# Kernel tuning notes

Measured on AMD Instinct MI355X. Metric: run time of the kernel, lower is better.

The kernel has to match this reference:

```python
import jax, jax.numpy as jnp
import numpy as np

N_NODES = 100000
N_EDGES = 3200000
N_FEAT = 128
N_GRAPHS = 64


def setup_inputs() -> dict:
    key = jax.random.key(0)
    ks = jax.random.split(key, 8)
    x = jax.random.normal(ks[0], (N_NODES, N_FEAT), dtype=jnp.float32)
    edge_index = jax.random.randint(ks[1], (2, N_EDGES), 0, N_NODES, dtype=jnp.int64)
    batch = jnp.sort(jax.random.randint(ks[2], (N_NODES,), 0, N_GRAPHS, dtype=jnp.int64))
    # GCNConv weights (glorot-style scale) and biases
    W1 = jax.random.normal(ks[3], (N_FEAT, 32), dtype=jnp.float32) / np.sqrt(N_FEAT)
    b1 = jnp.zeros((32,), dtype=jnp.float32)
    W2 = jax.random.normal(ks[4], (32, 16), dtype=jnp.float32) / np.sqrt(32.0)
    b2 = jnp.zeros((16,), dtype=jnp.float32)
    lin_w = jax.random.normal(ks[5], (16, 1), dtype=jnp.float32) / np.sqrt(16.0)
    lin_b = jnp.zeros((1,), dtype=jnp.float32)
    return {"x": x, "edge_index": edge_index, "batch": batch,
            "W1": W1, "b1": b1, "W2": W2, "b2": b2,
            "lin_w": lin_w, "lin_b": lin_b}


def _gcn_conv(x, W, b, src, dst, deg_inv_sqrt, n_nodes):
    # transform first (fewer features downstream when out_dim < in_dim)
    xw = x @ W  # [N, out]
    norm = deg_inv_sqrt[src] * deg_inv_sqrt[dst]  # [E+N]
    msg = xw[src] * norm[:, None]  # gather + scale
    out = jax.ops.segment_sum(msg, dst, num_segments=n_nodes)  # scatter-add
    return out + b


def reference(x, edge_index, batch, W1, b1, W2, b2, lin_w, lin_b):
    n_nodes = x.shape[0]
    self_loop = jnp.arange(n_nodes, dtype=edge_index.dtype)
    src = jnp.concatenate([edge_index[0], self_loop])
    dst = jnp.concatenate([edge_index[1], self_loop])
    # symmetric GCN normalization with self-loops
    deg = jax.ops.segment_sum(jnp.ones_like(src, dtype=x.dtype), dst,
                              num_segments=n_nodes)
    deg_inv_sqrt = jnp.where(deg > 0, jax.lax.rsqrt(jnp.maximum(deg, 1.0)), 0.0)

    h = _gcn_conv(x, W1, b1, src, dst, deg_inv_sqrt, n_nodes)
    h = jax.nn.relu(h)
    # F.dropout with training=False (eval) is identity
    h = _gcn_conv(h, W2, b2, src, dst, deg_inv_sqrt, n_nodes)

    # global_mean_pool over batch index
    sums = jax.ops.segment_sum(h, batch, num_segments=N_GRAPHS)  # [G,16]
    cnts = jax.ops.segment_sum(jnp.ones((n_nodes,), dtype=h.dtype), batch,
                               num_segments=N_GRAPHS)
    pooled = sums / jnp.maximum(cnts, 1.0)[:, None]
    return pooled @ lin_w + lin_b  # [G,1]
```

## Files before the change

### kernel.cpp

```cpp
#include <hip/hip_runtime.h>

#define NN 100000
#define NE 3200000
#define NF 128
#define C1 32
#define C2 16
#define NG 64
#define BKT_SH 7
#define BKT_W  128
#define NBKT   782
#define CH     8192
#define NW     391
#define RSTR   784
#define MAPCAP 6400

#define OFF_BCNT  0
#define OFF_BST   1024
#define OFF_RUN   2048
#define OFF_ROW   308608
#define OFF_DIS   408624
#define OFF_POOL  508624
#define OFF_CNTF  509648
#define OFF_EDG   509712
#define OFF_XS1B  OFF_EDG
#define OFF_H1    (OFF_EDG + NE)
#define OFF_XS2B  (OFF_H1  + NN*C1)
#define OFF_H2    (OFF_XS2B + NN*8)
#define OFF_COL   (OFF_H2  + NN*C2)

__device__ __forceinline__ unsigned pack_bf2(float a, float b) {
    unsigned ua = __float_as_uint(a);
    unsigned ub = __float_as_uint(b);
    ua = (ua + 0x7fffu + ((ua >> 16) & 1u)) >> 16;
    ub = (ub + 0x7fffu + ((ub >> 16) & 1u)) & 0xffff0000u;
    return ua | ub;
}
__device__ __forceinline__ float2 unpack_bf2(unsigned u) {
    return make_float2(__uint_as_float(u << 16), __uint_as_float(u & 0xffff0000u));
}

__global__ __launch_bounds__(256) void k_part(
    const int* __restrict__ S, const int* __restrict__ D,
    unsigned* __restrict__ edgebuf, int* __restrict__ runstart,
    int* __restrict__ bcnt)
{
    __shared__ int lhist[1024];
    __shared__ int lstart[1024];
    __shared__ int lcur[NBKT];
    __shared__ int sd[256];
    __shared__ unsigned lsort[CH];
    const int w = blockIdx.x;
    const int t = threadIdx.x;
    const int e0 = w * CH;
    const int n = min(CH, NE - e0);

    for (int i = t; i < 1024; i += 256) lhist[i] = 0;
    __syncthreads();
    for (int i = t; i < n; i += 256)
        atomicAdd(&lhist[(unsigned)D[e0 + i] >> BKT_SH], 1);
    __syncthreads();
    for (int i = t; i < NBKT; i += 256) atomicAdd(&bcnt[i], lhist[i]);
    int c0 = lhist[t * 4 + 0], c1 = lhist[t * 4 + 1];
    int c2 = lhist[t * 4 + 2], c3 = lhist[t * 4 + 3];
    int ts = c0 + c1 + c2 + c3;
    sd[t] = ts;
    __syncthreads();
    for (int off = 1; off < 256; off <<= 1) {
        int v = (t >= off) ? sd[t - off] : 0;
        __syncthreads();
        sd[t] += v;
        __syncthreads();
    }
    int excl = sd[t] - ts;
    lstart[t * 4 + 0] = excl;
    lstart[t * 4 + 1] = excl + c0;
    lstart[t * 4 + 2] = excl + c0 + c1;
    lstart[t * 4 + 3] = excl + c0 + c1 + c2;
    __syncthreads();
    for (int i = t; i < 783; i += 256) runstart[w * RSTR + i] = lstart[i];
    for (int i = t; i < NBKT; i += 256) lcur[i] = lstart[i];
    __syncthreads();
    for (int i = t; i < n; i += 256) {
        int s = S[e0 + i], d = D[e0 + i];
        int pos = atomicAdd(&lcur[(unsigned)d >> BKT_SH], 1);
        lsort[pos] = ((unsigned)s << BKT_SH) | (unsigned)(d & (BKT_W - 1));
    }
    __syncthreads();
    for (int i = t; i < n; i += 256) edgebuf[e0 + i] = lsort[i];
}

__global__ __launch_bounds__(256) void k_bscan(const int* __restrict__ bcnt,
                                               int* __restrict__ bstart,
                                               int* __restrict__ rowstart) {
    __shared__ int sd[256];
    const int t = threadIdx.x;
    const int base = t * 4;
    int c0 = (base + 0 < NBKT) ? bcnt[base + 0] : 0;
    int c1 = (base + 1 < NBKT) ? bcnt[base + 1] : 0;
    int c2 = (base + 2 < NBKT) ? bcnt[base + 2] : 0;
    int c3 = (base + 3 < NBKT) ? bcnt[base + 3] : 0;
    int ts = c0 + c1 + c2 + c3;
    sd[t] = ts;
    __syncthreads();
    for (int off = 1; off < 256; off <<= 1) {
        int v = (t >= off) ? sd[t - off] : 0;
        __syncthreads();
        sd[t] += v;
        __syncthreads();
    }
    int excl = sd[t] - ts;
    if (base + 0 < 783) bstart[base + 0] = excl;
    if (base + 1 < 783) bstart[base + 1] = excl + c0;
    if (base + 2 < 783) bstart[base + 2] = excl + c0 + c1;
    if (base + 3 < 783) bstart[base + 3] = excl + c0 + c1 + c2;
    if (t == 0) rowstart[NN] = NE;
}

__global__ __launch_bounds__(256) void k_fillfused(
    const unsigned* __restrict__ edgebuf, const int* __restrict__ runstart,
    const int* __restrict__ bstart,
    int* __restrict__ rowstart, float* __restrict__ dis, int* __restrict__ colidx)
{
    __shared__ int rl[NW];
    __shared__ int pfx[NW];
    __shared__ int basea[NW];
    __shared__ unsigned short map[MAPCAP];
    __shared__ int lcnt[BKT_W];
    __shared__ int lcur[BKT_W];
    __shared__ int sd[256];
    const int b = blockIdx.x;
    const int t = threadIdx.x;
    const int bs = bstart[b];
    const int total = bstart[b + 1] - bs;

    for (int w = t; w < NW; w += 256) {
        int s0 = runstart[w * RSTR + b];
        int s1 = runstart[w * RSTR + b + 1];
        basea[w] = s0;
        rl[w] = s1 - s0;
    }
    if (t < BKT_W) lcnt[t] = 0;
    __syncthreads();
    {
        int w0 = t * 2;
        int c0 = (w0 < NW) ? rl[w0] : 0;
        int c1 = (w0 + 1 < NW) ? rl[w0 + 1] : 0;
        int ts = c0 + c1;
        sd[t] = ts;
        __syncthreads();
        for (int off = 1; off < 256; off <<= 1) {
            int v = (t >= off) ? sd[t - off] : 0;
            __syncthreads();
            sd[t] += v;
            __syncthreads();
        }
        int excl = sd[t] - ts;
        if (w0 < NW)     pfx[w0]     = excl;
        if (w0 + 1 < NW) pfx[w0 + 1] = excl + c0;
    }
    __syncthreads();
    for (int w = t; w < NW; w += 256) {
        int p = pfx[w], len = rl[w];
        basea[w] = w * CH + basea[w] - p;
        for (int i = 0; i < len; ++i) map[p + i] = (unsigned short)w;
    }
    __syncthreads();
    for (int j = t; j < total; j += 256) {
        unsigned p = edgebuf[basea[map[j]] + j];
        atomicAdd(&lcnt[p & (BKT_W - 1)], 1);
    }
    __syncthreads();
    if (t < BKT_W) lcur[t] = lcnt[t];
    __syncthreads();
    for (int off = 1; off < BKT_W; off <<= 1) {
        int v = (t < BKT_W && t >= off) ? lcur[t - off] : 0;
        __syncthreads();
        if (t < BKT_W) lcur[t] += v;
        __syncthreads();
    }
    if (t < BKT_W) {
        int excl = lcur[t] - lcnt[t];
        int node = b * BKT_W + t;
        if (node < NN) {
            rowstart[node] = bs + excl;
            dis[node] = rsqrtf((float)lcnt[t] + 1.0f);
        }
        lcur[t] = bs + excl;
    }
    __syncthreads();
    for (int j = t; j < total; j += 256) {
        unsigned p = edgebuf[basea[map[j]] + j];
        int pos = atomicAdd(&lcur[p & (BKT_W - 1)], 1);
        colidx[pos] = (int)(p >> BKT_SH);
    }
}

__global__ __launch_bounds__(256) void k_gemm1(
    const float* __restrict__ x, const float* __restrict__ W1,
    const float* __restrict__ dis, unsigned* __restrict__ xs1b)
{
    __shared__ float xls[128 * 33];
    __shared__ float wls[32 * 32];
    const int t = threadIdx.x;
    const int tc = t & 7;
    const int tr = t >> 3;
    const int base = blockIdx.x * 128;

    float a[4][4] = {};

    for (int k0 = 0; k0 < NF; k0 += 32) {
        {
            int i = t * 4;
            int kk = i >> 5, c = i & 31;
            *(float4*)&wls[kk * 32 + c] = *(const float4*)&W1[(k0 + kk) * C1 + c];
        }
        #pragma unroll
        for (int r = 0; r < 4; ++r) {
            int n = (t >> 3) + r * 32;
            int j = (t & 7) * 4;
            int node = base + n;
            float4 v = make_float4(0.f, 0.f, 0.f, 0.f);
            if (node < NN) v = *(const float4*)&x[(long long)node * NF + k0 + j];
            xls[n * 33 + j + 0] = v.x;
            xls[n * 33 + j + 1] = v.y;
            xls[n * 33 + j + 2] = v.z;
            xls[n * 33 + j + 3] = v.w;
        }
        __syncthreads();
        #pragma unroll 8
        for (int kk = 0; kk < 32; ++kk) {
            float4 w = *(const float4*)&wls[kk * 32 + tc * 4];
            #pragma unroll
            for (int i = 0; i < 4; ++i) {
                float xv = xls[(tr * 4 + i) * 33 + kk];
                a[i][0] = fmaf(xv, w.x, a[i][0]);
                a[i][1] = fmaf(xv, w.y, a[i][1]);
                a[i][2] = fmaf(xv, w.z, a[i][2]);
                a[i][3] = fmaf(xv, w.w, a[i][3]);
            }
        }
        __syncthreads();
    }
    #pragma unroll
    for (int i = 0; i < 4; ++i) {
        int node = base + tr * 4 + i;
        if (node < NN) {
            float dv = dis[node];
            uint2 o;
            o.x = pack_bf2(a[i][0] * dv, a[i][1] * dv);
            o.y = pack_bf2(a[i][2] * dv, a[i][3] * dv);
            *(uint2*)&xs1b[node * 16 + tc * 2] = o;
        }
    }
}

__global__ __launch_bounds__(256) void k_gather1(
    const unsigned* __restrict__ xs1b, const int* __restrict__ colidx,
    const int* __restrict__ rowstart, const float* __restrict__ dis,
    const float* __restrict__ b1, float* __restrict__ h1)
{
    const int l = threadIdx.x & 15;
    const int v = blockIdx.x * 16 + (threadIdx.x >> 4);
    if (v >= NN) return;
    const int start = rowstart[v];
    const int num = rowstart[v + 1] - start;
    const int* __restrict__ cp = &colidx[start];

    float2 a0 = unpack_bf2(xs1b[v * 16 + l]);
    float2 a1 = make_float2(0.f, 0.f), a2 = a1, a3 = a1;
    int i = 0;
    for (; i + 4 <= num; i += 4) {
        int s0 = cp[i], s1 = cp[i + 1], s2 = cp[i + 2], s3 = cp[i + 3];
        float2 u0 = unpack_bf2(xs1b[s0 * 16 + l]);
        float2 u1 = unpack_bf2(xs1b[s1 * 16 + l]);
        float2 u2 = unpack_bf2(xs1b[s2 * 16 + l]);
        float2 u3 = unpack_bf2(xs1b[s3 * 16 + l]);
        a0.x += u0.x; a0.y += u0.y;
        a1.x += u1.x; a1.y += u1.y;
        a2.x += u2.x; a2.y += u2.y;
        a3.x += u3.x; a3.y += u3.y;
    }
    for (; i < num; ++i) {
        float2 u = unpack_bf2(xs1b[cp[i] * 16 + l]);
        a0.x += u.x; a0.y += u.y;
    }
    float accx = (a0.x + a1.x) + (a2.x + a3.x);
    float accy = (a0.y + a1.y) + (a2.y + a3.y);
    float dv = dis[v];
    float2 bv = *(const float2*)&b1[l * 2];
    float2 o;
    o.x = fmaxf(fmaf(accx, dv, bv.x), 0.f);
    o.y = fmaxf(fmaf(accy, dv, bv.y), 0.f);
    *(float2*)&h1[v * C1 + l * 2] = o;
}

__global__ __launch_bounds__(256) void k_gemm2(
    const float* __restrict__ h1, const float* __restrict__ W2,
    const float* __restrict__ dis, unsigned* __restrict__ xs2b)
{
    __shared__ float hls[128 * 33];
    __shared__ float wls[32 * 16];
    const int t = threadIdx.x;
    const int base = blockIdx.x * 128;

    if (t < 128) *(float4*)&wls[t * 4] = *(const float4*)&W2[t * 4];

    #pragma unroll
    for (int r = 0; r < 4; ++r) {
        int n = (t >> 3) + r * 32;
        int j = (t & 7) * 4;
        int node = base + n;
        float4 v = make_float4(0.f, 0.f, 0.f, 0.f);
        if (node < NN) v = *(const float4*)&h1[node * C1 + j];
        hls[n * 33 + j + 0] = v.x;
        hls[n * 33 + j + 1] = v.y;
        hls[n * 33 + j + 2] = v.z;
        hls[n * 33 + j + 3] = v.w;
    }
    __syncthreads();

    const int tc = t & 3;
    const int tr = t >> 2;
    float a[2][4] = {};
    #pragma unroll 8
    for (int kk = 0; kk < 32; ++kk) {
        float4 w = *(const float4*)&wls[kk * C2 + tc * 4];
        #pragma unroll
        for (int i = 0; i < 2; ++i) {
            float xv = hls[(tr * 2 + i) * 33 + kk];
            a[i][0] = fmaf(xv, w.x, a[i][0]);
            a[i][1] = fmaf(xv, w.y, a[i][1]);
            a[i][2] = fmaf(xv, w.z, a[i][2]);
            a[i][3] = fmaf(xv, w.w, a[i][3]);
        }
    }
    #pragma unroll
    for (int i = 0; i < 2; ++i) {
        int node = base + tr * 2 + i;
        if (node < NN) {
            float dv = dis[node];
            uint2 o;
            o.x = pack_bf2(a[i][0] * dv, a[i][1] * dv);
            o.y = pack_bf2(a[i][2] * dv, a[i][3] * dv);
            *(uint2*)&xs2b[node * 8 + tc * 2] = o;
        }
    }
}

__global__ __launch_bounds__(256) void k_gather2(
    const unsigned* __restrict__ xs2b, const int* __restrict__ colidx,
    const int* __restrict__ rowstart, const float* __restrict__ dis,
    const float* __restrict__ b2, float* __restrict__ h2)
{
    const int l = threadIdx.x & 7;
    const int v = blockIdx.x * 32 + (threadIdx.x >> 3);
    if (v >= NN) return;
    const int start = rowstart[v];
    const int num = rowstart[v + 1] - start;
    const int* __restrict__ cp = &colidx[start];

    float2 a0 = unpack_bf2(xs2b[v * 8 + l]);
    float2 a1 = make_float2(0.f, 0.f), a2 = a1, a3 = a1;
    int i = 0;
    for (; i + 4 <= num; i += 4) {
        int s0 = cp[i], s1 = cp[i + 1], s2 = cp[i + 2], s3 = cp[i + 3];
        float2 u0 = unpack_bf2(xs2b[s0 * 8 + l]);
        float2 u1 = unpack_bf2(xs2b[s1 * 8 + l]);
        float2 u2 = unpack_bf2(xs2b[s2 * 8 + l]);
        float2 u3 = unpack_bf2(xs2b[s3 * 8 + l]);
        a0.x += u0.x; a0.y += u0.y;
        a1.x += u1.x; a1.y += u1.y;
        a2.x += u2.x; a2.y += u2.y;
        a3.x += u3.x; a3.y += u3.y;
    }
    for (; i < num; ++i) {
        float2 u = unpack_bf2(xs2b[cp[i] * 8 + l]);
        a0.x += u.x; a0.y += u.y;
    }
    float accx = (a0.x + a1.x) + (a2.x + a3.x);
    float accy = (a0.y + a1.y) + (a2.y + a3.y);
    float dv = dis[v];
    float2 bv = *(const float2*)&b2[l * 2];
    float2 o;
    o.x = fmaf(accx, dv, bv.x);
    o.y = fmaf(accy, dv, bv.y);
    *(float2*)&h2[v * C2 + l * 2] = o;
}

__global__ __launch_bounds__(256) void k_pool(
    const float* __restrict__ h2, const int* __restrict__ batch,
    float* __restrict__ pool, float* __restrict__ cntf)
{
    __shared__ float ps[NG * C2];
    __shared__ float cs[NG];
    const int t = threadIdx.x;
    for (int i = t; i < NG * C2; i += 256) ps[i] = 0.f;
    if (t < NG) cs[t] = 0.f;
    __syncthreads();

    int v = blockIdx.x * 256 + t;
    if (v < NN) {
        int g = batch[v];
        atomicAdd(&cs[g], 1.0f);
        #pragma unroll
        for (int c = 0; c < C2; ++c)
            atomicAdd(&ps[g * C2 + c], h2[v * C2 + c]);
    }
    __syncthreads();
    for (int i = t; i < NG * C2; i += 256)
        if (ps[i] != 0.f) atomicAdd(&pool[i], ps[i]);
    if (t < NG && cs[t] != 0.f) atomicAdd(&cntf[t], cs[t]);
}

__global__ void k_final(const float* __restrict__ pool, const float* __restrict__ cntf,
                        const float* __restrict__ lw, const float* __restrict__ lb,
                        float* __restrict__ out)
{
    int g = threadIdx.x;
    if (g < NG) {
        float c = fmaxf(cntf[g], 1.0f);
        float inv = 1.0f / c;
        float s = lb[0];
        #pragma unroll
        for (int k = 0; k < C2; ++k) s = fmaf(pool[g * C2 + k] * inv, lw[k], s);
        out[g] = s;
    }
}

extern "C" void kernel_launch(void* const* d_in, const int* in_sizes, int n_in,
                              void* d_out, int out_size, void* d_ws, size_t ws_size,
                              hipStream_t stream) {
    const float* x     = (const float*)d_in[0];
    const int*   ei    = (const int*)d_in[1];
    const int*   batch = (const int*)d_in[2];
    const float* W1    = (const float*)d_in[3];
    const float* b1    = (const float*)d_in[4];
    const float* W2    = (const float*)d_in[5];
    const float* b2    = (const float*)d_in[6];
    const float* lw    = (const float*)d_in[7];
    const float* lb    = (const float*)d_in[8];
    float* out = (float*)d_out;

    float*    wsf = (float*)d_ws;
    int*      wsi = (int*)d_ws;
    unsigned* wsu = (unsigned*)d_ws;

    int*      bcnt     = wsi + OFF_BCNT;
    int*      bstart   = wsi + OFF_BST;
    int*      runstart = wsi + OFF_RUN;
    int*      rowstart = wsi + OFF_ROW;
    float*    dis      = wsf + OFF_DIS;
    float*    pool     = wsf + OFF_POOL;
    float*    cntf     = wsf + OFF_CNTF;
    unsigned* edgebuf  = wsu + OFF_EDG;
    unsigned* xs1b     = wsu + OFF_XS1B;
    float*    h1       = wsf + OFF_H1;
    unsigned* xs2b     = wsu + OFF_XS2B;
    float*    h2       = wsf + OFF_H2;
    int*      colidx   = wsi + OFF_COL;

    const int* S = ei;
    const int* D = ei + NE;

    hipMemsetAsync(bcnt, 0, 1024 * sizeof(int), stream);
    hipMemsetAsync(pool, 0, (NG * C2 + NG) * sizeof(float), stream);

    k_part     <<<NW, 256, 0, stream>>>(S, D, edgebuf, runstart, bcnt);
    k_bscan    <<<1, 256, 0, stream>>>(bcnt, bstart, rowstart);
    k_fillfused<<<NBKT, 256, 0, stream>>>(edgebuf, runstart, bstart, rowstart, dis, colidx);
    k_gemm1    <<<(NN + 127) / 128, 256, 0, stream>>>(x, W1, dis, xs1b);
    k_gather1  <<<(NN + 15) / 16, 256, 0, stream>>>(xs1b, colidx, rowstart, dis, b1, h1);
    k_gemm2    <<<(NN + 127) / 128, 256, 0, stream>>>(h1, W2, dis, xs2b);
    k_gather2  <<<(NN + 31) / 32, 256, 0, stream>>>(xs2b, colidx, rowstart, dis, b2, h2);
    k_pool     <<<(NN + 255) / 256, 256, 0, stream>>>(h2, batch, pool, cntf);
    k_final    <<<1, 64, 0, stream>>>(pool, cntf, lw, lb, out);
}
```

Before: 296.4 us.

## Split layer-1 gather into feature halves and fuse pooling into layer-2 gather

Layer-1 transformed features are stored as two separate 16-channel bf16 arrays, and the gather runs as two passes, each touching a 3.2 MB table instead of a 6.4 MB one. The aim is to keep the randomly gathered working set resident in cache. The cost is reading the column index list twice. Separately, the layer-2 gather now accumulates straight into shared-memory pooling sums, which removes the h2 buffer and the separate pool kernel at the price of more shared atomics inside the gather.

```diff
diff --git a/kernel.cpp b/kernel.cpp
--- a/kernel.cpp
+++ b/kernel.cpp
@@ -22,11 +22,12 @@
 #define OFF_POOL  508624
 #define OFF_CNTF  509648
 #define OFF_EDG   509712
-#define OFF_XS1B  OFF_EDG
-#define OFF_H1    (OFF_EDG + NE)
-#define OFF_XS2B  (OFF_H1  + NN*C1)
-#define OFF_H2    (OFF_XS2B + NN*8)
-#define OFF_COL   (OFF_H2  + NN*C2)
+#define OFF_XS1H0 OFF_EDG
+#define OFF_XS1H1 (OFF_EDG + NN*8)
+#define OFF_H1A   (OFF_EDG + NE)
+#define OFF_H1B   (OFF_H1A + NN*16)
+#define OFF_XS2B  (OFF_H1B + NN*16)
+#define OFF_COL   (OFF_XS2B + NN*8)
 
 __device__ __forceinline__ unsigned pack_bf2(float a, float b) {
     unsigned ua = __float_as_uint(a);
@@ -197,7 +198,8 @@
 
 __global__ __launch_bounds__(256) void k_gemm1(
     const float* __restrict__ x, const float* __restrict__ W1,
-    const float* __restrict__ dis, unsigned* __restrict__ xs1b)
+    const float* __restrict__ dis,
+    unsigned* __restrict__ xs1h0, unsigned* __restrict__ xs1h1)
 {
     __shared__ float xls[128 * 33];
     __shared__ float wls[32 * 32];
@@ -249,53 +251,57 @@
             uint2 o;
             o.x = pack_bf2(a[i][0] * dv, a[i][1] * dv);
             o.y = pack_bf2(a[i][2] * dv, a[i][3] * dv);
-            *(uint2*)&xs1b[node * 16 + tc * 2] = o;
-        }
-    }
-}
-
-__global__ __launch_bounds__(256) void k_gather1(
-    const unsigned* __restrict__ xs1b, const int* __restrict__ colidx,
+            unsigned* dst = (tc < 4) ? &xs1h0[node * 8 + tc * 2]
+                                     : &xs1h1[node * 8 + (tc - 4) * 2];
+            *(uint2*)dst = o;
+        }
+    }
+}
+
+template<int HALF>
+__global__ __launch_bounds__(256) void k_gather1h(
+    const unsigned* __restrict__ xsh, const int* __restrict__ colidx,
     const int* __restrict__ rowstart, const float* __restrict__ dis,
-    const float* __restrict__ b1, float* __restrict__ h1)
-{
-    const int l = threadIdx.x & 15;
-    const int v = blockIdx.x * 16 + (threadIdx.x >> 4);
+    const float* __restrict__ b1, float* __restrict__ h1h)
+{
+    const int l = threadIdx.x & 7;
+    const int v = blockIdx.x * 32 + (threadIdx.x >> 3);
     if (v >= NN) return;
     const int start = rowstart[v];
     const int num = rowstart[v + 1] - start;
     const int* __restrict__ cp = &colidx[start];
 
-    float2 a0 = unpack_bf2(xs1b[v * 16 + l]);
+    float2 a0 = unpack_bf2(xsh[v * 8 + l]);
     float2 a1 = make_float2(0.f, 0.f), a2 = a1, a3 = a1;
     int i = 0;
     for (; i + 4 <= num; i += 4) {
         int s0 = cp[i], s1 = cp[i + 1], s2 = cp[i + 2], s3 = cp[i + 3];
-        float2 u0 = unpack_bf2(xs1b[s0 * 16 + l]);
-        float2 u1 = unpack_bf2(xs1b[s1 * 16 + l]);
-        float2 u2 = unpack_bf2(xs1b[s2 * 16 + l]);
-        float2 u3 = unpack_bf2(xs1b[s3 * 16 + l]);
+        float2 u0 = unpack_bf2(xsh[s0 * 8 + l]);
+        float2 u1 = unpack_bf2(xsh[s1 * 8 + l]);
+        float2 u2 = unpack_bf2(xsh[s2 * 8 + l]);
+        float2 u3 = unpack_bf2(xsh[s3 * 8 + l]);
         a0.x += u0.x; a0.y += u0.y;
         a1.x += u1.x; a1.y += u1.y;
         a2.x += u2.x; a2.y += u2.y;
         a3.x += u3.x; a3.y += u3.y;
     }
     for (; i < num; ++i) {
-        float2 u = unpack_bf2(xs1b[cp[i] * 16 + l]);
+        float2 u = unpack_bf2(xsh[cp[i] * 8 + l]);
         a0.x += u.x; a0.y += u.y;
     }
     float accx = (a0.x + a1.x) + (a2.x + a3.x);
     float accy = (a0.y + a1.y) + (a2.y + a3.y);
     float dv = dis[v];
-    float2 bv = *(const float2*)&b1[l * 2];
+    float2 bv = *(const float2*)&b1[HALF * 16 + l * 2];
     float2 o;
     o.x = fmaxf(fmaf(accx, dv, bv.x), 0.f);
     o.y = fmaxf(fmaf(accy, dv, bv.y), 0.f);
-    *(float2*)&h1[v * C1 + l * 2] = o;
+    *(float2*)&h1h[v * 16 + l * 2] = o;
 }
 
 __global__ __launch_bounds__(256) void k_gemm2(
-    const float* __restrict__ h1, const float* __restrict__ W2,
+    const float* __restrict__ h1a, const float* __restrict__ h1b,
+    const float* __restrict__ W2,
     const float* __restrict__ dis, unsigned* __restrict__ xs2b)
 {
     __shared__ float hls[128 * 33];
@@ -311,7 +317,10 @@
         int j = (t & 7) * 4;
         int node = base + n;
         float4 v = make_float4(0.f, 0.f, 0.f, 0.f);
-        if (node < NN) v = *(const float4*)&h1[node * C1 + j];
+        if (node < NN) {
+            v = (j < 16) ? *(const float4*)&h1a[node * 16 + j]
+                         : *(const float4*)&h1b[node * 16 + (j - 16)];
+        }
         hls[n * 33 + j + 0] = v.x;
         hls[n * 33 + j + 1] = v.y;
         hls[n * 33 + j + 2] = v.z;
@@ -350,65 +359,53 @@
 __global__ __launch_bounds__(256) void k_gather2(
     const unsigned* __restrict__ xs2b, const int* __restrict__ colidx,
     const int* __restrict__ rowstart, const float* __restrict__ dis,
-    const float* __restrict__ b2, float* __restrict__ h2)
-{
-    const int l = threadIdx.x & 7;
-    const int v = blockIdx.x * 32 + (threadIdx.x >> 3);
-    if (v >= NN) return;
-    const int start = rowstart[v];
-    const int num = rowstart[v + 1] - start;
-    const int* __restrict__ cp = &colidx[start];
-
-    float2 a0 = unpack_bf2(xs2b[v * 8 + l]);
-    float2 a1 = make_float2(0.f, 0.f), a2 = a1, a3 = a1;
-    int i = 0;
-    for (; i + 4 <= num; i += 4) {
-        int s0 = cp[i], s1 = cp[i + 1], s2 = cp[i + 2], s3 = cp[i + 3];
-        float2 u0 = unpack_bf2(xs2b[s0 * 8 + l]);
-        float2 u1 = unpack_bf2(xs2b[s1 * 8 + l]);
-        float2 u2 = unpack_bf2(xs2b[s2 * 8 + l]);
-        float2 u3 = unpack_bf2(xs2b[s3 * 8 + l]);
-        a0.x += u0.x; a0.y += u0.y;
-        a1.x += u1.x; a1.y += u1.y;
-        a2.x += u2.x; a2.y += u2.y;
-        a3.x += u3.x; a3.y += u3.y;
-    }
-    for (; i < num; ++i) {
-        float2 u = unpack_bf2(xs2b[cp[i] * 8 + l]);
-        a0.x += u.x; a0.y += u.y;
-    }
-    float accx = (a0.x + a1.x) + (a2.x + a3.x);
-    float accy = (a0.y + a1.y) + (a2.y + a3.y);
-    float dv = dis[v];
-    float2 bv = *(const float2*)&b2[l * 2];
-    float2 o;
-    o.x = fmaf(accx, dv, bv.x);
-    o.y = fmaf(accy, dv, bv.y);
-    *(float2*)&h2[v * C2 + l * 2] = o;
-}
-
-__global__ __launch_bounds__(256) void k_pool(
-    const float* __restrict__ h2, const int* __restrict__ batch,
+    const float* __restrict__ b2, const int* __restrict__ batch,
     float* __restrict__ pool, float* __restrict__ cntf)
 {
-    __shared__ float ps[NG * C2];
+    __shared__ float psum[NG * C2];
     __shared__ float cs[NG];
     const int t = threadIdx.x;
-    for (int i = t; i < NG * C2; i += 256) ps[i] = 0.f;
+    for (int i = t; i < NG * C2; i += 256) psum[i] = 0.f;
     if (t < NG) cs[t] = 0.f;
     __syncthreads();
 
-    int v = blockIdx.x * 256 + t;
+    const int l = t & 7;
+    const int v = blockIdx.x * 32 + (t >> 3);
     if (v < NN) {
+        const int start = rowstart[v];
+        const int num = rowstart[v + 1] - start;
+        const int* __restrict__ cp = &colidx[start];
+
+        float2 a0 = unpack_bf2(xs2b[v * 8 + l]);
+        float2 a1 = make_float2(0.f, 0.f), a2 = a1, a3 = a1;
+        int i = 0;
+        for (; i + 4 <= num; i += 4) {
+            int s0 = cp[i], s1 = cp[i + 1], s2 = cp[i + 2], s3 = cp[i + 3];
+            float2 u0 = unpack_bf2(xs2b[s0 * 8 + l]);
+            float2 u1 = unpack_bf2(xs2b[s1 * 8 + l]);
+            float2 u2 = unpack_bf2(xs2b[s2 * 8 + l]);
+            float2 u3 = unpack_bf2(xs2b[s3 * 8 + l]);
+            a0.x += u0.x; a0.y += u0.y;
+            a1.x += u1.x; a1.y += u1.y;
+            a2.x += u2.x; a2.y += u2.y;
+            a3.x += u3.x; a3.y += u3.y;
+        }
+        for (; i < num; ++i) {
+            float2 u = unpack_bf2(xs2b[cp[i] * 8 + l]);
+            a0.x += u.x; a0.y += u.y;
+        }
+        float accx = (a0.x + a1.x) + (a2.x + a3.x);
+        float accy = (a0.y + a1.y) + (a2.y + a3.y);
+        float dv = dis[v];
+        float2 bv = *(const float2*)&b2[l * 2];
         int g = batch[v];
-        atomicAdd(&cs[g], 1.0f);
-        #pragma unroll
-        for (int c = 0; c < C2; ++c)
-            atomicAdd(&ps[g * C2 + c], h2[v * C2 + c]);
+        atomicAdd(&psum[g * C2 + l * 2],     fmaf(accx, dv, bv.x));
+        atomicAdd(&psum[g * C2 + l * 2 + 1], fmaf(accy, dv, bv.y));
+        if (l == 0) atomicAdd(&cs[g], 1.0f);
     }
     __syncthreads();
     for (int i = t; i < NG * C2; i += 256)
-        if (ps[i] != 0.f) atomicAdd(&pool[i], ps[i]);
+        if (psum[i] != 0.f) atomicAdd(&pool[i], psum[i]);
     if (t < NG && cs[t] != 0.f) atomicAdd(&cntf[t], cs[t]);
 }
 
@@ -453,10 +450,11 @@
     float*    pool     = wsf + OFF_POOL;
     float*    cntf     = wsf + OFF_CNTF;
     unsigned* edgebuf  = wsu + OFF_EDG;
-    unsigned* xs1b     = wsu + OFF_XS1B;
-    float*    h1       = wsf + OFF_H1;
+    unsigned* xs1h0    = wsu + OFF_XS1H0;
+    unsigned* xs1h1    = wsu + OFF_XS1H1;
+    float*    h1a      = wsf + OFF_H1A;
+    float*    h1b      = wsf + OFF_H1B;
     unsigned* xs2b     = wsu + OFF_XS2B;
-    float*    h2       = wsf + OFF_H2;
     int*      colidx   = wsi + OFF_COL;
 
     const int* S = ei;
@@ -465,13 +463,13 @@
     hipMemsetAsync(bcnt, 0, 1024 * sizeof(int), stream);
     hipMemsetAsync(pool, 0, (NG * C2 + NG) * sizeof(float), stream);
 
-    k_part     <<<NW, 256, 0, stream>>>(S, D, edgebuf, runstart, bcnt);
-    k_bscan    <<<1, 256, 0, stream>>>(bcnt, bstart, rowstart);
-    k_fillfused<<<NBKT, 256, 0, stream>>>(edgebuf, runstart, bstart, rowstart, dis, colidx);
-    k_gemm1    <<<(NN + 127) / 128, 256, 0, stream>>>(x, W1, dis, xs1b);
-    k_gather1  <<<(NN + 15) / 16, 256, 0, stream>>>(xs1b, colidx, rowstart, dis, b1, h1);
-    k_gemm2    <<<(NN + 127) / 128, 256, 0, stream>>>(h1, W2, dis, xs2b);
-    k_gather2  <<<(NN + 31) / 32, 256, 0, stream>>>(xs2b, colidx, rowstart, dis, b2, h2);
-    k_pool     <<<(NN + 255) / 256, 256, 0, stream>>>(h2, batch, pool, cntf);
-    k_final    <<<1, 64, 0, stream>>>(pool, cntf, lw, lb, out);
-}
+    k_part      <<<NW, 256, 0, stream>>>(S, D, edgebuf, runstart, bcnt);
+    k_bscan     <<<1, 256, 0, stream>>>(bcnt, bstart, rowstart);
+    k_fillfused <<<NBKT, 256, 0, stream>>>(edgebuf, runstart, bstart, rowstart, dis, colidx);
+    k_gemm1     <<<(NN + 127) / 128, 256, 0, stream>>>(x, W1, dis, xs1h0, xs1h1);
+    k_gather1h<0><<<(NN + 31) / 32, 256, 0, stream>>>(xs1h0, colidx, rowstart, dis, b1, h1a);
+    k_gather1h<1><<<(NN + 31) / 32, 256, 0, stream>>>(xs1h1, colidx, rowstart, dis, b1, h1b);
+    k_gemm2     <<<(NN + 127) / 128, 256, 0, stream>>>(h1a, h1b, W2, dis, xs2b);
+    k_gather2   <<<(NN + 31) / 32, 256, 0, stream>>>(xs2b, colidx, rowstart, dis, b2, batch, pool, cntf);
+    k_final     <<<1, 64, 0, stream>>>(pool, cntf, lw, lb, out);
+}
```

Measured after the change: 304.0 us. +2.6%, slower.
